# Kernel optimization log

Measured on AMD Instinct MI355X. Metric: run time of the kernel, lower is better.

Reference implementation:

```python
import jax, jax.numpy as jnp
import numpy as np

K = 128           # top-k
NUM_SAMPLES = 500 # perturbation samples
SIGMA = 0.05      # noise scale (forward arg sigma in the torch module)


def setup_inputs() -> dict:
    key = jax.random.key(0)
    k1, k2 = jax.random.split(key)
    x = jax.random.normal(k1, (32, 2048), dtype=jnp.float32)
    noise = jax.random.normal(k2, (32, NUM_SAMPLES, 2048), dtype=jnp.float32)
    return {"x": x, "noise": noise}


def reference(x, noise):
    # x: (b, d) scores; noise: (b, n, d) standard-normal perturbations.
    b, d = x.shape
    n = noise.shape[1]
    perturbed = x[:, None, :] + noise * SIGMA          # (b, n, d)
    _, idx = jax.lax.top_k(perturbed, K)               # (b, n, K) indices into d
    idx = jnp.sort(idx, axis=-1)                       # sorted, matching torch.sort
    # indicators[b,j,d] = mean_n one_hot(idx[b,n,j], d)
    # Computed with a scatter-add instead of materializing the (b,n,K,d) one-hot.
    bi = jnp.arange(b)[:, None, None]                  # (b,1,1)
    ki = jnp.arange(K)[None, None, :]                  # (1,1,K)
    counts = jnp.zeros((b, K, d), dtype=x.dtype).at[bi, ki, idx].add(1.0)
    indicators = counts / n                            # (b, K, d)
    return indicators, idx
```

## Files before the change

kernel.cpp:

```cpp
#include <hip/hip_runtime.h>


constexpr int B_     = 32;
constexpr int D_     = 2048;
constexpr int NS_    = 500;
constexpr int TOPK_  = 128;
constexpr float SIGMA_  = 0.05f;
constexpr float MARGIN_ = 0.25f;
constexpr int PER_LANE_ = D_ / 64;
constexpr int WAVES_PER_BLOCK_ = 4;
constexpr int CAP_   = 256;
constexpr int SLOTS_ = CAP_ / 64;
constexpr int JCHUNK_ = 8;

__device__ __forceinline__ uint32_t order_key(float f) {
  uint32_t u = __float_as_uint(f);
  return (u & 0x80000000u) ? ~u : (u | 0x80000000u);
}
__device__ __forceinline__ float inv_key(uint32_t k) {
  uint32_t u = (k & 0x80000000u) ? (k & 0x7FFFFFFFu) : ~k;
  return __uint_as_float(u);
}

__global__ __launch_bounds__(64) void ptk_cutoff(const float* __restrict__ x,
                                                 float* __restrict__ cutf) {
  const int lane = threadIdx.x & 63;
  const int b = blockIdx.x;
  const float* __restrict__ xr = x + (size_t)b * D_;
  uint32_t keys[PER_LANE_];
#pragma unroll
  for (int j = 0; j < PER_LANE_; j += 4) {
    const float4 xv = *reinterpret_cast<const float4*>(xr + lane * PER_LANE_ + j);
    keys[j + 0] = order_key(xv.x); keys[j + 1] = order_key(xv.y);
    keys[j + 2] = order_key(xv.z); keys[j + 3] = order_key(xv.w);
  }
  uint32_t prefix = 0; int k = TOPK_;
#pragma unroll 1
  for (int bit = 31; bit >= 0; --bit) {
    const uint32_t want = (prefix >> bit) | 1u;
    int c = 0;
#pragma unroll
    for (int j = 0; j < PER_LANE_; ++j) c += ((keys[j] >> bit) == want) ? 1 : 0;
#pragma unroll
    for (int off = 32; off >= 1; off >>= 1) c += __shfl_xor(c, off);
    if (c >= k) prefix |= (1u << bit); else k -= c;
  }
  if (lane == 0) cutf[b] = inv_key(prefix) - MARGIN_;
}

__global__ __launch_bounds__(256) void ptk_select(
    const float* __restrict__ x, const float* __restrict__ noise,
    const float* __restrict__ cutf, float* __restrict__ out_idx) {
  __shared__ uint2 comp[WAVES_PER_BLOCK_][CAP_];

  const int lane = threadIdx.x & 63;
  const int wave = threadIdx.x >> 6;
  const int row  = blockIdx.x * WAVES_PER_BLOCK_ + wave;
  const int b = row / NS_;
  const int n = row - b * NS_;

  const float* __restrict__ xr = x + (size_t)b * D_;
  const float* __restrict__ nr = noise + ((size_t)b * NS_ + n) * D_;
  const int base_i = lane * PER_LANE_;

  float p[PER_LANE_];
#pragma unroll
  for (int j = 0; j < PER_LANE_; j += 4) {
    const float4 nv = *reinterpret_cast<const float4*>(nr + base_i + j);
    const float4 xv = *reinterpret_cast<const float4*>(xr + base_i + j);
    p[j + 0] = fmaf(SIGMA_, nv.x, xv.x);
    p[j + 1] = fmaf(SIGMA_, nv.y, xv.y);
    p[j + 2] = fmaf(SIGMA_, nv.z, xv.z);
    p[j + 3] = fmaf(SIGMA_, nv.w, xv.w);
  }

  const float cf = cutf[b];

  uint32_t m = 0;
#pragma unroll
  for (int j = 0; j < PER_LANE_; ++j) m |= (p[j] >= cf) ? (1u << j) : 0u;
  const int cnt = __popc(m);

  const uint64_t below = (lane == 0) ? 0ull : ((~0ull) >> (64 - lane));
  int offset = 0, C = 0;
#pragma unroll
  for (int t = 0; t < 6; ++t) {
    const uint64_t mb = __ballot((cnt >> t) & 1);
    offset += (int)__popcll(mb & below) << t;
    C      += (int)__popcll(mb) << t;
  }

  float* __restrict__ idx_row = out_idx + (size_t)row * TOPK_;

  if (C >= TOPK_ && C <= CAP_) {
    {
      uint32_t mm = m; int q = offset;
      while (mm) {
        const int j = __ffs(mm) - 1; mm &= mm - 1;
        comp[wave][q] = make_uint2(order_key(p[j]), (uint32_t)(base_i + j));
        ++q;
      }
    }
    __asm__ volatile("s_waitcnt lgkmcnt(0)" ::: "memory");

    uint32_t kk[SLOTS_], ki[SLOTS_];
    bool valid[SLOTS_];
#pragma unroll
    for (int s = 0; s < SLOTS_; ++s) {
      const int q = (s << 6) + lane;
      valid[s] = (q < C);
      const uint2 v = valid[s] ? comp[wave][q] : make_uint2(0u, 0u);
      kk[s] = v.x; ki[s] = v.y;
    }

    uint32_t orv = 0u, andv = 0xFFFFFFFFu;
#pragma unroll
    for (int s = 0; s < SLOTS_; ++s) {
      orv  |= valid[s] ? kk[s] : 0u;
      andv &= valid[s] ? kk[s] : 0xFFFFFFFFu;
    }
#pragma unroll
    for (int off = 32; off >= 1; off >>= 1) {
      orv  |= __shfl_xor(orv, off);
      andv &= __shfl_xor(andv, off);
    }
    const uint32_t diff = orv ^ andv;

    uint32_t prefix; int r;
    if (diff == 0u) {
      prefix = orv; r = TOPK_;
    } else {
      const int startbit = 31 - __clz(diff);
      prefix = (startbit == 31) ? 0u : (andv & (0xFFFFFFFFu << (startbit + 1)));
      int k = TOPK_;
      int A = C;
#pragma unroll 1
      for (int bit = startbit; bit >= 0; --bit) {
        const uint32_t want = (prefix >> bit) | 1u;
        int c = 0;
#pragma unroll
        for (int s = 0; s < SLOTS_; ++s)
          c += __popcll(__ballot((kk[s] >> bit) == want));
        if (c >= k) { prefix |= (1u << bit); A = c; }
        else        { k -= c; A -= c; }
        if (A == 1) {
          uint32_t mykey = 0u; bool have = false;
#pragma unroll
          for (int s = 0; s < SLOTS_; ++s) {
            const bool hit = valid[s] && ((kk[s] >> bit) == (prefix >> bit));
            mykey = hit ? kk[s] : mykey;
            have |= hit;
          }
          const uint64_t mb = __ballot(have);
          const int src = __ffsll((unsigned long long)mb) - 1;
          prefix = __shfl(mykey, src);
          k = 1;
          break;
        }
      }
      r = k;
    }

    int sel_run = 0, eq_run = 0;
#pragma unroll
    for (int s = 0; s < SLOTS_; ++s) {
      const bool gt = kk[s] > prefix;
      const bool eq = kk[s] == prefix;
      const uint64_t meq = __ballot(eq);
      const int eqrank = eq_run + __popcll(meq & below);
      const bool sel = gt || (eq && (eqrank < r));
      const uint64_t msel = __ballot(sel);
      if (sel) {
        const int pos = sel_run + __popcll(msel & below);
        idx_row[pos] = (float)(int)ki[s];
      }
      sel_run += __popcll(msel);
      eq_run  += __popcll(meq);
    }
  } else {
    uint32_t keys[PER_LANE_];
#pragma unroll
    for (int j = 0; j < PER_LANE_; ++j) keys[j] = order_key(p[j]);

    uint32_t prefix = 0; int k = TOPK_;
#pragma unroll 1
    for (int bit = 31; bit >= 0; --bit) {
      const uint32_t want = (prefix >> bit) | 1u;
      int c = 0;
#pragma unroll
      for (int j = 0; j < PER_LANE_; ++j) c += ((keys[j] >> bit) == want) ? 1 : 0;
#pragma unroll
      for (int off = 32; off >= 1; off >>= 1) c += __shfl_xor(c, off);
      if (c >= k) prefix |= (1u << bit); else k -= c;
    }
    const int r = k;

    int gt = 0, eq = 0;
#pragma unroll
    for (int j = 0; j < PER_LANE_; ++j) {
      gt += (keys[j] > prefix) ? 1 : 0;
      eq += (keys[j] == prefix) ? 1 : 0;
    }
    uint32_t incl2 = (uint32_t)gt | ((uint32_t)eq << 16);
#pragma unroll
    for (int off = 1; off < 64; off <<= 1) {
      uint32_t y = __shfl_up(incl2, (unsigned)off);
      if (lane >= off) incl2 += y;
    }
    const int gt_base = (int)(incl2 & 0xFFFFu) - gt;
    const int eq_base = (int)(incl2 >> 16) - eq;
    int pos = gt_base + min(eq_base, r);
    int eq_seen = eq_base;
#pragma unroll
    for (int j = 0; j < PER_LANE_; ++j) {
      const uint32_t kj = keys[j];
      bool s = false;
      if (kj > prefix) s = true;
      else if (kj == prefix) { s = (eq_seen < r); eq_seen++; }
      if (s) { idx_row[pos] = (float)(base_i + j); pos++; }
    }
  }
}

__global__ __launch_bounds__(256) void ptk_hist(
    const float* __restrict__ out_idx, float* __restrict__ indicators) {
  __shared__ int hist[JCHUNK_][D_];

  const int tid   = threadIdx.x;
  const int b     = blockIdx.x >> 4;
  const int chunk = blockIdx.x & 15;
  const int j0    = chunk * JCHUNK_;

  int4* h4 = (int4*)hist;
  for (int t = tid; t < JCHUNK_ * D_ / 4; t += 256)
    h4[t] = make_int4(0, 0, 0, 0);
  __syncthreads();

  const float* __restrict__ src = out_idx + (size_t)b * NS_ * TOPK_ + j0;
  for (int t = tid; t < NS_ * 2; t += 256) {
    const int n = t >> 1;
    const int q = (t & 1) << 2;
    const float4 v = *reinterpret_cast<const float4*>(src + (size_t)n * TOPK_ + q);
    atomicAdd(&hist[q + 0][(int)v.x], 1);
    atomicAdd(&hist[q + 1][(int)v.y], 1);
    atomicAdd(&hist[q + 2][(int)v.z], 1);
    atomicAdd(&hist[q + 3][(int)v.w], 1);
  }
  __syncthreads();

  float4* __restrict__ dst =
      (float4*)(indicators + ((size_t)b * TOPK_ + j0) * D_);
  for (int t = tid; t < JCHUNK_ * D_ / 4; t += 256) {
    const int4 h = h4[t];
    float4 o;
    o.x = (float)h.x / (float)NS_;
    o.y = (float)h.y / (float)NS_;
    o.z = (float)h.z / (float)NS_;
    o.w = (float)h.w / (float)NS_;
    dst[t] = o;
  }
}

extern "C" void kernel_launch(void* const* d_in, const int* in_sizes, int n_in,
                              void* d_out, int out_size, void* d_ws, size_t ws_size,
                              hipStream_t stream) {
  const float* x     = (const float*)d_in[0];
  const float* noise = (const float*)d_in[1];
  float* indicators  = (float*)d_out;
  float* out_idx     = (float*)d_out + (size_t)B_ * TOPK_ * D_;
  float* cutf        = (float*)d_ws;

  hipLaunchKernelGGL(ptk_cutoff, dim3(B_), dim3(64), 0, stream, x, cutf);

  const int rows = B_ * NS_;
  hipLaunchKernelGGL(ptk_select, dim3(rows / WAVES_PER_BLOCK_), dim3(256), 0,
                     stream, x, noise, cutf, out_idx);

  hipLaunchKernelGGL(ptk_hist, dim3(B_ * 16), dim3(256), 0, stream,
                     out_idx, indicators);
}
```

Before: 234.9 us.

## Use lane-interleaved float4 loads and per-chunk ballot compaction for candidate selection

Each lane now reads the noise and x rows as float4 at stride 64, so a wave's loads are fully coalesced, instead of each lane reading a contiguous 32-float block. Because of that the element a lane owns changes. Candidate compaction is rebuilt as a per-quad ballot prefix sum so the shared-memory compacted list stays in ascending index order. The fallback path reloads the original contiguous layout from global memory, which adds extra reads in that rare case. The intent is to cut memory transaction overhead on the dominant noise-streaming load, at the cost of more ballots (24 instead of 6).

New measurement: 252.4 us. +7.5%, slower.

```diff
diff --git a/kernel.cpp b/kernel.cpp
--- a/kernel.cpp
+++ b/kernel.cpp
@@ -8,6 +8,7 @@
 constexpr float SIGMA_  = 0.05f;
 constexpr float MARGIN_ = 0.25f;
 constexpr int PER_LANE_ = D_ / 64;
+constexpr int NQ_    = PER_LANE_ / 4;
 constexpr int WAVES_PER_BLOCK_ = 4;
 constexpr int CAP_   = 256;
 constexpr int SLOTS_ = CAP_ / 64;
@@ -57,47 +58,60 @@
   const int wave = threadIdx.x >> 6;
   const int row  = blockIdx.x * WAVES_PER_BLOCK_ + wave;
   const int b = row / NS_;
-  const int n = row - b * NS_;
-
-  const float* __restrict__ xr = x + (size_t)b * D_;
-  const float* __restrict__ nr = noise + ((size_t)b * NS_ + n) * D_;
-  const int base_i = lane * PER_LANE_;
+
+  const float4* __restrict__ xr4 =
+      reinterpret_cast<const float4*>(x + (size_t)b * D_);
+  const float4* __restrict__ nr4 =
+      reinterpret_cast<const float4*>(noise + (size_t)row * D_);
+
+  float4 nv[NQ_], xv[NQ_];
+#pragma unroll
+  for (int j = 0; j < NQ_; ++j) nv[j] = nr4[(j << 6) + lane];
+#pragma unroll
+  for (int j = 0; j < NQ_; ++j) xv[j] = xr4[(j << 6) + lane];
 
   float p[PER_LANE_];
 #pragma unroll
-  for (int j = 0; j < PER_LANE_; j += 4) {
-    const float4 nv = *reinterpret_cast<const float4*>(nr + base_i + j);
-    const float4 xv = *reinterpret_cast<const float4*>(xr + base_i + j);
-    p[j + 0] = fmaf(SIGMA_, nv.x, xv.x);
-    p[j + 1] = fmaf(SIGMA_, nv.y, xv.y);
-    p[j + 2] = fmaf(SIGMA_, nv.z, xv.z);
-    p[j + 3] = fmaf(SIGMA_, nv.w, xv.w);
+  for (int j = 0; j < NQ_; ++j) {
+    p[4 * j + 0] = fmaf(SIGMA_, nv[j].x, xv[j].x);
+    p[4 * j + 1] = fmaf(SIGMA_, nv[j].y, xv[j].y);
+    p[4 * j + 2] = fmaf(SIGMA_, nv[j].z, xv[j].z);
+    p[4 * j + 3] = fmaf(SIGMA_, nv[j].w, xv[j].w);
   }
 
   const float cf = cutf[b];
 
   uint32_t m = 0;
 #pragma unroll
-  for (int j = 0; j < PER_LANE_; ++j) m |= (p[j] >= cf) ? (1u << j) : 0u;
-  const int cnt = __popc(m);
+  for (int t = 0; t < PER_LANE_; ++t) m |= (p[t] >= cf) ? (1u << t) : 0u;
 
   const uint64_t below = (lane == 0) ? 0ull : ((~0ull) >> (64 - lane));
-  int offset = 0, C = 0;
-#pragma unroll
-  for (int t = 0; t < 6; ++t) {
-    const uint64_t mb = __ballot((cnt >> t) & 1);
-    offset += (int)__popcll(mb & below) << t;
-    C      += (int)__popcll(mb) << t;
-  }
+  int pre[NQ_], tot[NQ_];
+#pragma unroll
+  for (int j = 0; j < NQ_; ++j) {
+    const int cnt = __popc((m >> (4 * j)) & 0xFu);
+    const uint64_t b0 = __ballot(cnt & 1);
+    const uint64_t b1 = __ballot(cnt & 2);
+    const uint64_t b2 = __ballot(cnt & 4);
+    pre[j] = (int)__popcll(b0 & below) + 2 * (int)__popcll(b1 & below) +
+             4 * (int)__popcll(b2 & below);
+    tot[j] = (int)__popcll(b0) + 2 * (int)__popcll(b1) + 4 * (int)__popcll(b2);
+  }
+  int jbase[NQ_]; int C = 0;
+#pragma unroll
+  for (int j = 0; j < NQ_; ++j) { jbase[j] = C; C += tot[j]; }
 
   float* __restrict__ idx_row = out_idx + (size_t)row * TOPK_;
 
   if (C >= TOPK_ && C <= CAP_) {
-    {
-      uint32_t mm = m; int q = offset;
-      while (mm) {
-        const int j = __ffs(mm) - 1; mm &= mm - 1;
-        comp[wave][q] = make_uint2(order_key(p[j]), (uint32_t)(base_i + j));
+#pragma unroll
+    for (int j = 0; j < NQ_; ++j) {
+      uint32_t nib = (m >> (4 * j)) & 0xFu;
+      int q = jbase[j] + pre[j];
+      while (nib) {
+        const int c = __ffs(nib) - 1; nib &= nib - 1;
+        comp[wave][q] = make_uint2(order_key(p[4 * j + c]),
+                                   (uint32_t)((j << 8) + (lane << 2) + c));
         ++q;
       }
     }
@@ -178,9 +192,13 @@
       eq_run  += __popcll(meq);
     }
   } else {
+    const float* __restrict__ xr = x + (size_t)b * D_;
+    const float* __restrict__ nr = noise + (size_t)row * D_;
+    const int base_i = lane * PER_LANE_;
     uint32_t keys[PER_LANE_];
 #pragma unroll
-    for (int j = 0; j < PER_LANE_; ++j) keys[j] = order_key(p[j]);
+    for (int j = 0; j < PER_LANE_; ++j)
+      keys[j] = order_key(fmaf(SIGMA_, nr[base_i + j], xr[base_i + j]));
 
     uint32_t prefix = 0; int k = TOPK_;
 #pragma unroll 1
```
